# Kernel optimization log

Measured on AMD Instinct MI355X. Metric: run time of the kernel, lower is better.

Reference implementation:

```python
import jax, jax.numpy as jnp
import numpy as np

N_EDGES = 500_000
D = 64            # per-tensor feature dim
N_GRAPHS = 1024
IN_DIM = 4 * D    # 256
H = 64            # hidden dims (64, 64)


def setup_inputs() -> dict:
    key = jax.random.key(0)
    k = jax.random.split(key, 9)
    src = jax.random.normal(k[0], (N_EDGES, D), dtype=jnp.float32)
    dest = jax.random.normal(k[1], (N_EDGES, D), dtype=jnp.float32)
    edge_attr = jax.random.normal(k[2], (N_EDGES, D), dtype=jnp.float32)
    u = jax.random.normal(k[3], (N_GRAPHS, D), dtype=jnp.float32)
    batch = jax.random.randint(k[4], (N_EDGES,), 0, N_GRAPHS, dtype=jnp.int64)
    # MLP params: Linear(256->64) -> ReLU -> Linear(64->64) -> ReLU  (dropout_rate=0.0)
    s1 = 1.0 / np.sqrt(IN_DIM)
    s2 = 1.0 / np.sqrt(H)
    W1 = jax.random.uniform(k[5], (IN_DIM, H), jnp.float32, -s1, s1)
    b1 = jax.random.uniform(k[6], (H,), jnp.float32, -s1, s1)
    W2 = jax.random.uniform(k[7], (H, H), jnp.float32, -s2, s2)
    b2 = jax.random.uniform(k[8], (H,), jnp.float32, -s2, s2)
    return {"src": src, "dest": dest, "edge_attr": edge_attr, "u": u,
            "batch": batch, "W1": W1, "b1": b1, "W2": W2, "b2": b2}


def reference(src, dest, edge_attr, u, batch, W1, b1, W2, b2):
    # gather global state per edge and concat: [E, 4*D]
    comb = jnp.concatenate([src, dest, edge_attr, u[batch]], axis=1)
    h = jax.nn.relu(comb @ W1 + b1)   # dropout_rate=0.0 -> identity
    out = jax.nn.relu(h @ W2 + b2)
    return out
```

## Files before the change

kernel.cpp:

```cpp
#include <hip/hip_runtime.h>
#include <cstdint>
#include <cstddef>

typedef __attribute__((ext_vector_type(8))) short short8;
typedef __attribute__((ext_vector_type(4))) float f32x4;

__device__ __forceinline__ unsigned short f2bf(float f) {
    union { float f; unsigned int u; } v;
    v.f = f;
    unsigned int r = v.u + 0x7fffu + ((v.u >> 16) & 1u);
    return (unsigned short)(r >> 16);
}

#define HPAD 72

__device__ __forceinline__ int bswz(int k, int n) {
    const int ks = k >> 5, quad = (k >> 3) & 3, j = k & 7;
    const int nt = n >> 4, lo = n & 15;
    return ((((ks << 2) + nt) << 6) + (quad << 4) + lo) * 8 + j;
}

__global__ __launch_bounds__(512, 4)
void megnet_edge(const float* __restrict__ g_src,
                 const float* __restrict__ g_dst,
                 const float* __restrict__ g_ea,
                 const float* __restrict__ g_u,
                 const int*   __restrict__ g_batch,
                 const float* __restrict__ g_W1,
                 const float* __restrict__ g_b1,
                 const float* __restrict__ g_W2,
                 const float* __restrict__ g_b2,
                 float* __restrict__ g_out,
                 int E, int NG, int ntiles)
{
    __shared__ unsigned short w1s[256 * 64];
    __shared__ unsigned short w2s[64 * 64];
    __shared__ unsigned short hbuf[8][32 * HPAD];

    const int tid = threadIdx.x;

    for (int i = tid; i < 4096; i += 512) {
        const int flat = i << 2;
        const int k = flat >> 6, n0 = flat & 63;
        const float* p = g_W1 + flat;
        #pragma unroll
        for (int c = 0; c < 4; ++c)
            w1s[bswz(k, n0 + c)] = f2bf(p[c]);
    }
    for (int i = tid; i < 1024; i += 512) {
        const int flat = i << 2;
        const int k = flat >> 6, n0 = flat & 63;
        const float* p = g_W2 + flat;
        #pragma unroll
        for (int c = 0; c < 4; ++c)
            w2s[bswz(k, n0 + c)] = f2bf(p[c]);
    }
    __syncthreads();

    const int lane = tid & 63;
    const int wave = tid >> 6;
    const int lo   = lane & 15;
    const int quad = lane >> 4;
    const short8* w1f = (const short8*)w1s;
    const short8* w2f = (const short8*)w2s;
    unsigned short* hw = &hbuf[wave][0];

    float bias1[4], bias2[4];
    #pragma unroll
    for (int nt = 0; nt < 4; ++nt) {
        bias1[nt] = g_b1[(nt << 4) + lo];
        bias2[nt] = g_b2[(nt << 4) + lo];
    }

    for (int tile = blockIdx.x; tile < ntiles; tile += gridDim.x) {
        const int e_base = tile * 256 + wave * 32;

        const float* pseg[2][4];
        #pragma unroll
        for (int mt = 0; mt < 2; ++mt) {
            const int row = e_base + (mt << 4) + lo;
            const int rc  = row < E ? row : E - 1;
            pseg[mt][0] = g_src + (size_t)rc * 64;
            pseg[mt][1] = g_dst + (size_t)rc * 64;
            pseg[mt][2] = g_ea  + (size_t)rc * 64;
            int g = g_batch[rc];
            g = g < 0 ? 0 : (g >= NG ? NG - 1 : g);
            pseg[mt][3] = g_u + (size_t)g * 64;
        }

        f32x4 acc[2][4];
        #pragma unroll
        for (int mt = 0; mt < 2; ++mt)
            #pragma unroll
            for (int nt = 0; nt < 4; ++nt)
                acc[mt][nt] = (f32x4){0.f, 0.f, 0.f, 0.f};

        float4 ld[2][2][2];
        auto issue = [&](int ks, int buf) {
            const int seg = ks >> 1;
            const int co  = ((ks & 1) << 5) + (quad << 3);
            #pragma unroll
            for (int mt = 0; mt < 2; ++mt) {
                const float* p = pseg[mt][seg] + co;
                ld[buf][mt][0] = *reinterpret_cast<const float4*>(p);
                ld[buf][mt][1] = *reinterpret_cast<const float4*>(p + 4);
            }
        };
        issue(0, 0);
        issue(1, 1);

        #pragma unroll
        for (int ks = 0; ks < 8; ++ks) {
            short8 afrag[2];
            #pragma unroll
            for (int mt = 0; mt < 2; ++mt) {
                const float4 x = ld[ks & 1][mt][0];
                const float4 y = ld[ks & 1][mt][1];
                short8 t;
                t[0] = (short)f2bf(x.x); t[1] = (short)f2bf(x.y);
                t[2] = (short)f2bf(x.z); t[3] = (short)f2bf(x.w);
                t[4] = (short)f2bf(y.x); t[5] = (short)f2bf(y.y);
                t[6] = (short)f2bf(y.z); t[7] = (short)f2bf(y.w);
                afrag[mt] = t;
            }
            if (ks < 6) issue(ks + 2, ks & 1);
            #pragma unroll
            for (int nt = 0; nt < 4; ++nt) {
                const short8 b = w1f[(((ks << 2) + nt) << 6) + lane];
                #pragma unroll
                for (int mt = 0; mt < 2; ++mt)
                    acc[mt][nt] = __builtin_amdgcn_mfma_f32_16x16x32_bf16(
                        afrag[mt], b, acc[mt][nt], 0, 0, 0);
            }
        }

        #pragma unroll
        for (int nt = 0; nt < 4; ++nt) {
            const int col = (nt << 4) + lo;
            #pragma unroll
            for (int mt = 0; mt < 2; ++mt) {
                #pragma unroll
                for (int r = 0; r < 4; ++r) {
                    float v = acc[mt][nt][r] + bias1[nt];
                    v = v > 0.f ? v : 0.f;
                    hw[((mt << 4) + (quad << 2) + r) * HPAD + col] = f2bf(v);
                }
            }
        }

        f32x4 acc2[2][4];
        #pragma unroll
        for (int mt = 0; mt < 2; ++mt)
            #pragma unroll
            for (int nt = 0; nt < 4; ++nt)
                acc2[mt][nt] = (f32x4){0.f, 0.f, 0.f, 0.f};

        #pragma unroll
        for (int ks = 0; ks < 2; ++ks) {
            short8 afrag[2];
            #pragma unroll
            for (int mt = 0; mt < 2; ++mt) {
                const unsigned short* hp =
                    hw + ((mt << 4) + lo) * HPAD + (ks << 5) + (quad << 3);
                afrag[mt] = *reinterpret_cast<const short8*>(hp);
            }
            #pragma unroll
            for (int nt = 0; nt < 4; ++nt) {
                const short8 b = w2f[(((ks << 2) + nt) << 6) + lane];
                #pragma unroll
                for (int mt = 0; mt < 2; ++mt)
                    acc2[mt][nt] = __builtin_amdgcn_mfma_f32_16x16x32_bf16(
                        afrag[mt], b, acc2[mt][nt], 0, 0, 0);
            }
        }

        #pragma unroll
        for (int mt = 0; mt < 2; ++mt) {
            #pragma unroll
            for (int r = 0; r < 4; ++r) {
                const int row = e_base + (mt << 4) + (quad << 2) + r;
                if (row < E) {
                    float* op = g_out + (size_t)row * 64;
                    #pragma unroll
                    for (int nt = 0; nt < 4; ++nt) {
                        const int col = (nt << 4) + lo;
                        float v = acc2[mt][nt][r] + bias2[nt];
                        op[col] = v > 0.f ? v : 0.f;
                    }
                }
            }
        }
    }
}

extern "C" void kernel_launch(void* const* d_in, const int* in_sizes, int n_in,
                              void* d_out, int out_size, void* d_ws, size_t ws_size,
                              hipStream_t stream) {
    const float* g_src   = (const float*)d_in[0];
    const float* g_dst   = (const float*)d_in[1];
    const float* g_ea    = (const float*)d_in[2];
    const float* g_u     = (const float*)d_in[3];
    const int*   g_batch = (const int*)  d_in[4];
    const float* g_W1    = (const float*)d_in[5];
    const float* g_b1    = (const float*)d_in[6];
    const float* g_W2    = (const float*)d_in[7];
    const float* g_b2    = (const float*)d_in[8];
    float*       g_out   = (float*)d_out;

    const int E  = in_sizes[0] / 64;
    const int NG = in_sizes[3] / 64;
    const int ntiles = (E + 255) / 256;

    int grid = ntiles < 512 ? ntiles : 512;
    megnet_edge<<<grid, 512, 0, stream>>>(g_src, g_dst, g_ea, g_u, g_batch,
                                          g_W1, g_b1, g_W2, g_b2, g_out,
                                          E, NG, ntiles);
}
```

Baseline: 460.1 us.

## Keep hidden activations in registers via transposed MFMA and 16x16x16 second layer

```diff
diff --git a/kernel.cpp b/kernel.cpp
--- a/kernel.cpp
+++ b/kernel.cpp
@@ -3,7 +3,18 @@
 #include <cstddef>
 
 typedef __attribute__((ext_vector_type(8))) short short8;
+typedef __attribute__((ext_vector_type(4))) short short4v;
 typedef __attribute__((ext_vector_type(4))) float f32x4;
+
+#if !defined(__HIP_DEVICE_COMPILE__)
+  #define MFMA16(A, B, C) (C)
+#elif __has_builtin(__builtin_amdgcn_mfma_f32_16x16x16bf16_1k)
+  #define MFMA16(A, B, C) __builtin_amdgcn_mfma_f32_16x16x16bf16_1k((A), (B), (C), 0, 0, 0)
+#elif __has_builtin(__builtin_amdgcn_mfma_f32_16x16x16_bf16)
+  #define MFMA16(A, B, C) __builtin_amdgcn_mfma_f32_16x16x16_bf16((A), (B), (C), 0, 0, 0)
+#else
+  #error "no 16x16x16 bf16 MFMA builtin on device"
+#endif
 
 __device__ __forceinline__ unsigned short f2bf(float f) {
     union { float f; unsigned int u; } v;
@@ -12,30 +23,33 @@
     return (unsigned short)(r >> 16);
 }
 
-#define HPAD 72
-
 __device__ __forceinline__ int bswz(int k, int n) {
     const int ks = k >> 5, quad = (k >> 3) & 3, j = k & 7;
     const int nt = n >> 4, lo = n & 15;
     return ((((ks << 2) + nt) << 6) + (quad << 4) + lo) * 8 + j;
 }
 
-__global__ __launch_bounds__(512, 4)
-void megnet_edge(const float* __restrict__ g_src,
-                 const float* __restrict__ g_dst,
-                 const float* __restrict__ g_ea,
-                 const float* __restrict__ g_u,
-                 const int*   __restrict__ g_batch,
-                 const float* __restrict__ g_W1,
-                 const float* __restrict__ g_b1,
-                 const float* __restrict__ g_W2,
-                 const float* __restrict__ g_b2,
-                 float* __restrict__ g_out,
-                 int E, int NG, int ntiles)
+__device__ __forceinline__ int w2swz(int k, int n) {
+    const int ks2 = k >> 4, q = (k >> 2) & 3, j = k & 3;
+    const int nt2 = n >> 4, lo = n & 15;
+    return ((((ks2 << 2) + nt2) << 6) + (q << 4) + lo) * 4 + j;
+}
+
+__global__ void __attribute__((amdgpu_waves_per_eu(4, 6))) __launch_bounds__(512)
+megnet_edge(const float* __restrict__ g_src,
+            const float* __restrict__ g_dst,
+            const float* __restrict__ g_ea,
+            const float* __restrict__ g_u,
+            const int*   __restrict__ g_batch,
+            const float* __restrict__ g_W1,
+            const float* __restrict__ g_b1,
+            const float* __restrict__ g_W2,
+            const float* __restrict__ g_b2,
+            float* __restrict__ g_out,
+            int E, int NG, int ntiles)
 {
     __shared__ unsigned short w1s[256 * 64];
     __shared__ unsigned short w2s[64 * 64];
-    __shared__ unsigned short hbuf[8][32 * HPAD];
 
     const int tid = threadIdx.x;
 
@@ -53,7 +67,7 @@
         const float* p = g_W2 + flat;
         #pragma unroll
         for (int c = 0; c < 4; ++c)
-            w2s[bswz(k, n0 + c)] = f2bf(p[c]);
+            w2s[w2swz(k, n0 + c)] = f2bf(p[c]);
     }
     __syncthreads();
 
@@ -61,132 +75,109 @@
     const int wave = tid >> 6;
     const int lo   = lane & 15;
     const int quad = lane >> 4;
-    const short8* w1f = (const short8*)w1s;
-    const short8* w2f = (const short8*)w2s;
-    unsigned short* hw = &hbuf[wave][0];
-
-    float bias1[4], bias2[4];
-    #pragma unroll
-    for (int nt = 0; nt < 4; ++nt) {
-        bias1[nt] = g_b1[(nt << 4) + lo];
-        bias2[nt] = g_b2[(nt << 4) + lo];
-    }
+    const short8*  w1f = (const short8*)w1s;
+    const short4v* w2f = (const short4v*)w2s;
 
     for (int tile = blockIdx.x; tile < ntiles; tile += gridDim.x) {
         const int e_base = tile * 256 + wave * 32;
 
-        const float* pseg[2][4];
+        int off[2], uoff[2];
         #pragma unroll
         for (int mt = 0; mt < 2; ++mt) {
             const int row = e_base + (mt << 4) + lo;
             const int rc  = row < E ? row : E - 1;
-            pseg[mt][0] = g_src + (size_t)rc * 64;
-            pseg[mt][1] = g_dst + (size_t)rc * 64;
-            pseg[mt][2] = g_ea  + (size_t)rc * 64;
+            off[mt] = rc << 6;
             int g = g_batch[rc];
             g = g < 0 ? 0 : (g >= NG ? NG - 1 : g);
-            pseg[mt][3] = g_u + (size_t)g * 64;
+            uoff[mt] = g << 6;
         }
 
         f32x4 acc[2][4];
         #pragma unroll
-        for (int mt = 0; mt < 2; ++mt)
-            #pragma unroll
-            for (int nt = 0; nt < 4; ++nt)
-                acc[mt][nt] = (f32x4){0.f, 0.f, 0.f, 0.f};
-
-        float4 ld[2][2][2];
-        auto issue = [&](int ks, int buf) {
+        for (int nt = 0; nt < 4; ++nt) {
+            const float4 b = *reinterpret_cast<const float4*>(
+                g_b1 + (nt << 4) + (quad << 2));
+            acc[0][nt] = (f32x4){b.x, b.y, b.z, b.w};
+            acc[1][nt] = (f32x4){b.x, b.y, b.z, b.w};
+        }
+
+        #pragma unroll
+        for (int ks = 0; ks < 8; ++ks) {
             const int seg = ks >> 1;
             const int co  = ((ks & 1) << 5) + (quad << 3);
+            short8 xf[2];
             #pragma unroll
             for (int mt = 0; mt < 2; ++mt) {
-                const float* p = pseg[mt][seg] + co;
-                ld[buf][mt][0] = *reinterpret_cast<const float4*>(p);
-                ld[buf][mt][1] = *reinterpret_cast<const float4*>(p + 4);
-            }
-        };
-        issue(0, 0);
-        issue(1, 1);
-
-        #pragma unroll
-        for (int ks = 0; ks < 8; ++ks) {
-            short8 afrag[2];
-            #pragma unroll
-            for (int mt = 0; mt < 2; ++mt) {
-                const float4 x = ld[ks & 1][mt][0];
-                const float4 y = ld[ks & 1][mt][1];
+                const float* base = seg == 0 ? g_src
+                                  : seg == 1 ? g_dst
+                                  : seg == 2 ? g_ea : g_u;
+                const int o = (seg == 3 ? uoff[mt] : off[mt]) + co;
+                const float4 x = *reinterpret_cast<const float4*>(base + o);
+                const float4 y = *reinterpret_cast<const float4*>(base + o + 4);
                 short8 t;
                 t[0] = (short)f2bf(x.x); t[1] = (short)f2bf(x.y);
                 t[2] = (short)f2bf(x.z); t[3] = (short)f2bf(x.w);
                 t[4] = (short)f2bf(y.x); t[5] = (short)f2bf(y.y);
                 t[6] = (short)f2bf(y.z); t[7] = (short)f2bf(y.w);
-                afrag[mt] = t;
-            }
-            if (ks < 6) issue(ks + 2, ks & 1);
+                xf[mt] = t;
+            }
             #pragma unroll
             for (int nt = 0; nt < 4; ++nt) {
-                const short8 b = w1f[(((ks << 2) + nt) << 6) + lane];
+                const short8 a = w1f[(((ks << 2) + nt) << 6) + lane];
                 #pragma unroll
                 for (int mt = 0; mt < 2; ++mt)
                     acc[mt][nt] = __builtin_amdgcn_mfma_f32_16x16x32_bf16(
-                        afrag[mt], b, acc[mt][nt], 0, 0, 0);
-            }
-        }
-
-        #pragma unroll
-        for (int nt = 0; nt < 4; ++nt) {
-            const int col = (nt << 4) + lo;
-            #pragma unroll
-            for (int mt = 0; mt < 2; ++mt) {
+                        a, xf[mt], acc[mt][nt], 0, 0, 0);
+            }
+        }
+
+        short4v pa[2][4];
+        #pragma unroll
+        for (int mt = 0; mt < 2; ++mt) {
+            #pragma unroll
+            for (int nt = 0; nt < 4; ++nt) {
+                short4v t;
                 #pragma unroll
                 for (int r = 0; r < 4; ++r) {
-                    float v = acc[mt][nt][r] + bias1[nt];
+                    float v = acc[mt][nt][r];
                     v = v > 0.f ? v : 0.f;
-                    hw[((mt << 4) + (quad << 2) + r) * HPAD + col] = f2bf(v);
+                    t[r] = (short)f2bf(v);
                 }
+                pa[mt][nt] = t;
             }
         }
 
         f32x4 acc2[2][4];
         #pragma unroll
-        for (int mt = 0; mt < 2; ++mt)
-            #pragma unroll
-            for (int nt = 0; nt < 4; ++nt)
-                acc2[mt][nt] = (f32x4){0.f, 0.f, 0.f, 0.f};
-
-        #pragma unroll
-        for (int ks = 0; ks < 2; ++ks) {
-            short8 afrag[2];
-            #pragma unroll
-            for (int mt = 0; mt < 2; ++mt) {
-                const unsigned short* hp =
-                    hw + ((mt << 4) + lo) * HPAD + (ks << 5) + (quad << 3);
-                afrag[mt] = *reinterpret_cast<const short8*>(hp);
-            }
-            #pragma unroll
-            for (int nt = 0; nt < 4; ++nt) {
-                const short8 b = w2f[(((ks << 2) + nt) << 6) + lane];
+        for (int nt2 = 0; nt2 < 4; ++nt2) {
+            const float4 b = *reinterpret_cast<const float4*>(
+                g_b2 + (nt2 << 4) + (quad << 2));
+            acc2[0][nt2] = (f32x4){b.x, b.y, b.z, b.w};
+            acc2[1][nt2] = (f32x4){b.x, b.y, b.z, b.w};
+        }
+        #pragma unroll
+        for (int nt2 = 0; nt2 < 4; ++nt2) {
+            #pragma unroll
+            for (int ks2 = 0; ks2 < 4; ++ks2) {
+                const short4v a = w2f[(((ks2 << 2) + nt2) << 6) + lane];
+                acc2[0][nt2] = MFMA16(a, pa[0][ks2], acc2[0][nt2]);
+                acc2[1][nt2] = MFMA16(a, pa[1][ks2], acc2[1][nt2]);
+            }
+        }
+
+        #pragma unroll
+        for (int mt = 0; mt < 2; ++mt) {
+            const int row = e_base + (mt << 4) + lo;
+            if (row < E) {
+                float* op = g_out + (size_t)row * 64 + (quad << 2);
                 #pragma unroll
-                for (int mt = 0; mt < 2; ++mt)
-                    acc2[mt][nt] = __builtin_amdgcn_mfma_f32_16x16x32_bf16(
-                        afrag[mt], b, acc2[mt][nt], 0, 0, 0);
-            }
-        }
-
-        #pragma unroll
-        for (int mt = 0; mt < 2; ++mt) {
-            #pragma unroll
-            for (int r = 0; r < 4; ++r) {
-                const int row = e_base + (mt << 4) + (quad << 2) + r;
-                if (row < E) {
-                    float* op = g_out + (size_t)row * 64;
-                    #pragma unroll
-                    for (int nt = 0; nt < 4; ++nt) {
-                        const int col = (nt << 4) + lo;
-                        float v = acc2[mt][nt][r] + bias2[nt];
-                        op[col] = v > 0.f ? v : 0.f;
-                    }
+                for (int nt2 = 0; nt2 < 4; ++nt2) {
+                    float4 v;
+                    v.x = acc2[mt][nt2][0] > 0.f ? acc2[mt][nt2][0] : 0.f;
+                    v.y = acc2[mt][nt2][1] > 0.f ? acc2[mt][nt2][1] : 0.f;
+                    v.z = acc2[mt][nt2][2] > 0.f ? acc2[mt][nt2][2] : 0.f;
+                    v.w = acc2[mt][nt2][3] > 0.f ? acc2[mt][nt2][3] : 0.f;
+                    *reinterpret_cast<float4*>(op + (nt2 << 4)) = v;
                 }
             }
         }
@@ -211,7 +202,7 @@
     const int NG = in_sizes[3] / 64;
     const int ntiles = (E + 255) / 256;
 
-    int grid = ntiles < 512 ? ntiles : 512;
+    int grid = ntiles < 768 ? ntiles : 768;
     megnet_edge<<<grid, 512, 0, stream>>>(g_src, g_dst, g_ea, g_u, g_batch,
                                           g_W1, g_b1, g_W2, g_b2, g_out,
                                           E, NG, ntiles);
```

New measurement: 579.7 us. 1.26x slower.
